# Kernel optimization log

Measured on AMD Instinct MI355X. Metric: run time of the kernel, lower is better.

## Reference

```python
import jax, jax.numpy as jnp
import numpy as np

EPS = 1e-6
K = 20
B, N = 4, 4096
HID, CDIM = 128, 64


def vn_lin(W, x):
    # W: [Cout, Cin], x: [B, Cin, 3, ...] -> [B, Cout, 3, ...]
    return jnp.einsum('oc,bc...->bo...', W, x)


def vn_leaky(x, d, ns=0.0):
    # vector-neuron leaky ReLU: reflect the part of x anti-aligned with direction d
    dot = jnp.sum(x * d, axis=2, keepdims=True)
    dsq = jnp.sum(d * d, axis=2, keepdims=True)
    return ns * x + (1.0 - ns) * jnp.where(dot >= 0, x, x - (dot / (dsq + EPS)) * d)


def vn_max_pool(x, Wd):
    # pool over the LAST axis, picking per-(b,c) the vector maximizing <x, d>
    d = vn_lin(Wd, x)
    dot = jnp.sum(x * d, axis=2, keepdims=True)            # [B,C,1,...,L]
    idx = jnp.broadcast_to(jnp.argmax(dot, axis=-1), x.shape[:-1])
    return jnp.take_along_axis(x, idx[..., None], axis=-1)[..., 0]


def graph_feature_cross(pts, k):
    # pts: [B, N, 3] -> [B, 3ch, 3vec, N, k] with channels (nbr-x, x, cross(nbr,x))
    sq = jnp.sum(pts * pts, axis=-1)
    inner = jnp.einsum('bnd,bmd->bnm', pts, pts)
    neg_dist = 2.0 * inner - sq[:, :, None] - sq[:, None, :]
    _, idx = jax.lax.top_k(neg_dist, k)                     # [B, N, k]
    nbr = jax.vmap(lambda p, i: p[i])(pts, idx)             # [B, N, k, 3]
    x = jnp.broadcast_to(pts[:, :, None, :], nbr.shape)
    cross = jnp.cross(nbr, x, axis=-1)
    feat = jnp.stack([nbr - x, x, cross], axis=3)           # [B, N, k, 3ch, 3vec]
    return jnp.transpose(feat, (0, 3, 4, 1, 2))


def resblock(x, a0, f0, a1, f1, sc):
    net = vn_lin(f0, vn_leaky(x, vn_lin(a0, x)))
    dx = vn_lin(f1, vn_leaky(net, vn_lin(a1, net)))
    return vn_lin(sc, x) + dx


def _init(key, shape, fan_in):
    return jax.random.normal(key, shape, jnp.float32) / np.sqrt(fan_in)


def setup_inputs():
    key = jax.random.key(0)
    ks = jax.random.split(key, 14)
    return {
        'pc': jax.random.normal(ks[0], (B, N, 3), jnp.float32),
        'conv_Wf': _init(ks[1], (64, 3), 3),
        'conv_Wd': _init(ks[2], (64, 3), 3),
        'pool_pos_Wd': _init(ks[3], (64, 64), 64),
        'fc_pos_W': _init(ks[4], (2 * HID, 64), 64),
        'blk_a0': _init(ks[5], (5, 2 * HID, 2 * HID), 2 * HID),
        'blk_f0': _init(ks[6], (5, HID, 2 * HID), 2 * HID),
        'blk_a1': _init(ks[7], (5, HID, HID), HID),
        'blk_f1': _init(ks[8], (5, HID, HID), HID),
        'blk_sc': _init(ks[9], (5, HID, 2 * HID), 2 * HID),
        'pool_Wd': _init(ks[10], (5, HID, HID), HID),
        'actc_Wd': _init(ks[11], (HID, HID), HID),
        'fcc_W': _init(ks[12], (CDIM, HID), HID),
    }


def reference(pc, conv_Wf, conv_Wd, pool_pos_Wd, fc_pos_W, blk_a0, blk_f0, blk_a1, blk_f1, blk_sc, pool_Wd, actc_Wd, fcc_W):
    b = pc.shape[0]
    feat = graph_feature_cross(pc, K)                         # [B,3,3,N,k]
    net = vn_leaky(vn_lin(conv_Wf, feat), vn_lin(conv_Wd, feat))  # [B,64,3,N,k]
    net = vn_max_pool(net, pool_pos_Wd)                       # [B,64,3,N] (pool over k)
    net = vn_lin(fc_pos_W, net)                               # [B,256,3,N]
    for i in range(5):
        net = resblock(net, blk_a0[i], blk_f0[i], blk_a1[i], blk_f1[i], blk_sc[i])  # [B,128,3,N]
        if i < 4:
            pooled = vn_max_pool(net, pool_Wd[i])             # [B,128,3] (pool over N)
            net = jnp.concatenate([net, jnp.broadcast_to(pooled[..., None], net.shape)], axis=1)
    net = vn_max_pool(net, pool_Wd[4])                        # [B,128,3]
    c = vn_lin(fcc_W, vn_leaky(net, vn_lin(actc_Wd, net)))    # [B,64,3]
    return c.reshape(b, -1)                                   # [B,192]
```

## Files before the change

### kernel.cpp

```cpp
#include <hip/hip_runtime.h>
#include <hip/hip_bf16.h>
#include <math.h>

#define NPTS 4096
#define NB 4
#define KNN 20
#define NCOLS (3*NPTS)
#define NEG_INF (-__builtin_huge_valf())
#define DNEG_INF (-__builtin_huge_val())

typedef _Float16 f16x8 __attribute__((ext_vector_type(8)));
typedef _Float16 f16x4 __attribute__((ext_vector_type(4)));
typedef float f32x4 __attribute__((ext_vector_type(4)));

#define WOFF_FC 0
#define WOFF_A0 16384
#define WOFF_F0 344064
#define WOFF_A1 507904
#define WOFF_F1 589824
#define WOFF_SC 671744
#define WOFF_PW 835584
#define WTOT    917504

__global__ __launch_bounds__(512) void knn_kernel(const float* __restrict__ pc,
                                                  int* __restrict__ idx) {
  __shared__ float pts[NPTS*3];
  __shared__ double msv[2][8];
  __shared__ int    msn[2][8];
  int b = blockIdx.x >> 10;
  int rowblk = blockIdx.x & 1023;
  const float* pb = pc + (size_t)b*NPTS*3;
  for (int i = threadIdx.x; i < NPTS*3; i += 512) pts[i] = pb[i];
  __syncthreads();
  int wave = threadIdx.x >> 6;
  int lane = threadIdx.x & 63;
  int row  = wave >> 1;
  int half = wave & 1;
  int l128 = half*64 + lane;
  int n = rowblk*4 + row;
  double pn0 = pts[n*3+0], pn1 = pts[n*3+1], pn2 = pts[n*3+2];
  double sqn = pn0*pn0 + pn1*pn1 + pn2*pn2;
  double nd[32];
#pragma unroll
  for (int j = 0; j < 32; ++j) {
    int m = j*128 + l128;
    double q0 = pts[m*3+0], q1 = pts[m*3+1], q2 = pts[m*3+2];
    double inner = pn0*q0 + pn1*q1 + pn2*q2;
    double sqm = q0*q0 + q1*q1 + q2*q2;
    nd[j] = 2.0*inner - sqn - sqm;
  }
  double gm[2]; int gj[2];
#pragma unroll
  for (int g = 0; g < 2; ++g) {
    double v = nd[g*16]; int jb = g*16;
#pragma unroll
    for (int jj = 1; jj < 16; ++jj) {
      int j = g*16 + jj;
      bool take = nd[j] > v;
      v = take ? nd[j] : v;
      jb = take ? j : jb;
    }
    gm[g] = v; gj[g] = jb;
  }
  int* orow = idx + ((size_t)b*NPTS + n)*KNN;
  for (int t = 0; t < KNN; ++t) {
    double bv = gm[0]; int bj = gj[0];
    if (gm[1] > bv) { bv = gm[1]; bj = gj[1]; }
    int bm = bj*128 + l128;
#pragma unroll
    for (int s = 1; s < 64; s <<= 1) {
      double ov = __shfl_xor(bv, s, 64);
      int om = __shfl_xor(bm, s, 64);
      bool take = (ov > bv) || (ov == bv && om < bm);
      bv = take ? ov : bv;
      bm = take ? om : bm;
    }
    if (lane == 0) { msv[t&1][wave] = bv; msn[t&1][wave] = bm; }
    __syncthreads();
    {
      double pv = msv[t&1][wave^1]; int pm = msn[t&1][wave^1];
      bool take = (pv > bv) || (pv == bv && pm < bm);
      bv = take ? pv : bv;
      bm = take ? pm : bm;
    }
    if (half == 0 && lane == 0) orow[t] = bm;
    if (t < KNN-1) {
      int vic_l128 = bm & 127;
      int jw = bm >> 7;
      int vic_half = vic_l128 >> 6;
      if (vic_half == half) {
        bool iswl = (l128 == vic_l128);
        int gw = jw >> 4;
#define REBUILD(G) { \
  _Pragma("unroll") \
  for (int jj = 0; jj < 16; ++jj) { \
    int j = (G)*16 + jj; \
    if (iswl && j == jw) nd[j] = DNEG_INF; \
  } \
  double v = nd[(G)*16]; int jb = (G)*16; \
  _Pragma("unroll") \
  for (int jj = 1; jj < 16; ++jj) { \
    int j = (G)*16 + jj; \
    bool take = nd[j] > v; \
    v = take ? nd[j] : v; \
    jb = take ? j : jb; \
  } \
  gm[G] = v; gj[G] = jb; \
}
        if (gw == 0) REBUILD(0)
        else         REBUILD(1)
#undef REBUILD
      }
    }
  }
}

#define ECH 5
__global__ __launch_bounds__(128) void edgeconv_kernel(
    const float* __restrict__ pc, const int* __restrict__ knnidx,
    const float* __restrict__ Wf, const float* __restrict__ Wd,
    const float* __restrict__ Wp, float* __restrict__ outp) {
  __shared__ float xls[2*ECH*3*64];
  int wave = threadIdx.x >> 6, lane = threadIdx.x & 63;
  int pid0 = blockIdx.x * 2;
  int b = pid0 >> 12;
  int n = (pid0 & (NPTS-1)) + wave;
  const float* pb = pc + (size_t)b*NPTS*3;
  int c = lane;
  float wrow[64];
#pragma unroll
  for (int j = 0; j < 64; ++j) wrow[j] = Wp[c*64 + j];
  float wf0 = Wf[c*3+0], wf1 = Wf[c*3+1], wf2 = Wf[c*3+2];
  float wd0 = Wd[c*3+0], wd1 = Wd[c*3+1], wd2 = Wd[c*3+2];
  float f9[9];
#pragma unroll
  for (int i = 0; i < 9; ++i) f9[i] = 0.0f;
  if (lane < KNN) {
    int j = knnidx[((size_t)b*NPTS + n)*KNN + lane];
    float q0 = pb[j*3+0], q1 = pb[j*3+1], q2 = pb[j*3+2];
    float x0 = pb[n*3+0], x1 = pb[n*3+1], x2 = pb[n*3+2];
    f9[0] = q0-x0; f9[1] = q1-x1; f9[2] = q2-x2;
    f9[3] = x0;    f9[4] = x1;    f9[5] = x2;
    f9[6] = q1*x2 - q2*x1;
    f9[7] = q2*x0 - q0*x2;
    f9[8] = q0*x1 - q1*x0;
  }
  float* xw = &xls[wave*ECH*3*64];
  double bdot = DNEG_INF;
  float bx0 = 0.f, bx1 = 0.f, bx2 = 0.f;
  for (int k0 = 0; k0 < KNN; k0 += ECH) {
    for (int kc = 0; kc < ECH; ++kc) {
      int kk = k0 + kc;
      float fch[9];
#pragma unroll
      for (int i = 0; i < 9; ++i) fch[i] = __shfl(f9[i], kk, 64);
      float fv[3], dv[3];
#pragma unroll
      for (int v = 0; v < 3; ++v) {
        fv[v] = wf0*fch[v] + wf1*fch[3+v] + wf2*fch[6+v];
        dv[v] = wd0*fch[v] + wd1*fch[3+v] + wd2*fch[6+v];
      }
      float dot = fv[0]*dv[0] + fv[1]*dv[1] + fv[2]*dv[2];
      if (dot < 0.0f) {
        float dsq = dv[0]*dv[0] + dv[1]*dv[1] + dv[2]*dv[2];
        float s = dot / (dsq + 1e-6f);
        fv[0] -= s*dv[0]; fv[1] -= s*dv[1]; fv[2] -= s*dv[2];
      }
      xw[(0*ECH+kc)*64 + c] = fv[0];
      xw[(1*ECH+kc)*64 + c] = fv[1];
      xw[(2*ECH+kc)*64 + c] = fv[2];
    }
    for (int kc = 0; kc < ECH; ++kc) {
      float a0 = 0.f, a1 = 0.f, a2 = 0.f;
#pragma unroll
      for (int j = 0; j < 64; j += 4) {
        float4 v0 = *(const float4*)&xw[(0*ECH+kc)*64 + j];
        float4 v1 = *(const float4*)&xw[(1*ECH+kc)*64 + j];
        float4 v2 = *(const float4*)&xw[(2*ECH+kc)*64 + j];
        a0 += wrow[j]*v0.x + wrow[j+1]*v0.y + wrow[j+2]*v0.z + wrow[j+3]*v0.w;
        a1 += wrow[j]*v1.x + wrow[j+1]*v1.y + wrow[j+2]*v1.z + wrow[j+3]*v1.w;
        a2 += wrow[j]*v2.x + wrow[j+1]*v2.y + wrow[j+2]*v2.z + wrow[j+3]*v2.w;
      }
      float xc0 = xw[(0*ECH+kc)*64 + c];
      float xc1 = xw[(1*ECH+kc)*64 + c];
      float xc2 = xw[(2*ECH+kc)*64 + c];
      double dd = (double)xc0*a0 + (double)xc1*a1 + (double)xc2*a2;
      bool take = dd > bdot;
      bdot = take ? dd : bdot;
      bx0 = take ? xc0 : bx0;
      bx1 = take ? xc1 : bx1;
      bx2 = take ? xc2 : bx2;
    }
  }
  outp[((size_t)b*NCOLS + 0*NPTS + n)*64 + c] = bx0;
  outp[((size_t)b*NCOLS + 1*NPTS + n)*64 + c] = bx1;
  outp[((size_t)b*NCOLS + 2*NPTS + n)*64 + c] = bx2;
}

__global__ __launch_bounds__(256) void wsplit_kernel(
    const float* __restrict__ fc, const float* __restrict__ a0,
    const float* __restrict__ f0, const float* __restrict__ a1,
    const float* __restrict__ f1, const float* __restrict__ sc,
    const float* __restrict__ pw, _Float16* __restrict__ outp) {
  int i = blockIdx.x*256 + threadIdx.x;
  const float* src; int off;
  if      (i < WOFF_A0) { src = fc; off = WOFF_FC; }
  else if (i < WOFF_F0) { src = a0; off = WOFF_A0; }
  else if (i < WOFF_A1) { src = f0; off = WOFF_F0; }
  else if (i < WOFF_F1) { src = a1; off = WOFF_A1; }
  else if (i < WOFF_SC) { src = f1; off = WOFF_F1; }
  else if (i < WOFF_PW) { src = sc; off = WOFF_SC; }
  else                  { src = pw; off = WOFF_PW; }
  float w = src[i - off];
  _Float16 h = (_Float16)w;
  outp[i] = h;
  outp[i + WTOT] = (_Float16)(w - (float)h);
}

__global__ __launch_bounds__(256) void bias_kernel(
    const float* __restrict__ W, const float* __restrict__ pooled,
    float* __restrict__ bias, int Cout, int Wstride) {
  int id = blockIdx.x*256 + threadIdx.x;
  int co = id % Cout; int t = id / Cout;
  int v = t % 3; int b = t / 3;
  double acc = 0.0;
  const float* wr = W + (size_t)co*Wstride + 128;
  const float* pp = pooled + (size_t)b*384 + v;
#pragma unroll 4
  for (int c = 0; c < 128; ++c)
    acc += (double)wr[c] * (double)pp[c*3];
  bias[id] = (float)acc;
}

#define LDP 40
__global__ __launch_bounds__(256) void gemm_mfma(
    const _Float16* __restrict__ Wh, const _Float16* __restrict__ Wl,
    const float* __restrict__ X, const float* __restrict__ Z,
    const float* __restrict__ bias, float* __restrict__ Y,
    int Cin, int Wstride, int ldX, int ldY, int ldZ, int addZ, int Cbias) {
  __shared__ __align__(16) _Float16 Ah[64*LDP];
  __shared__ __align__(16) _Float16 Al[64*LDP];
  __shared__ __align__(16) _Float16 Bh[128*LDP];
  __shared__ __align__(16) _Float16 Bl[128*LDP];
  int b = blockIdx.z;
  int sp0 = blockIdx.x * 64;
  int co0 = blockIdx.y * 128;
  const float* Xb = X + ((size_t)b*NCOLS + sp0) * ldX;
  int t = threadIdx.x;
  int arow = t >> 2, akoff = (t & 3) * 8;
  int brow = t >> 1, bkoff = (t & 1) * 16;
  int wid = t >> 6, lane = t & 63;
  int wr = (wid >> 1) * 32, wc = (wid & 1) * 64;
  int lrow = lane & 15, lk = (lane >> 4) * 8;
  f32x4 acc[2][4];
#pragma unroll
  for (int f = 0; f < 2; ++f)
#pragma unroll
    for (int g = 0; g < 4; ++g)
#pragma unroll
      for (int r = 0; r < 4; ++r) acc[f][g][r] = 0.0f;

  for (int k0 = 0; k0 < Cin; k0 += 32) {
    const float* xs = Xb + (size_t)arow*ldX + k0 + akoff;
    float xv[8];
    *(float4*)&xv[0] = *(const float4*)&xs[0];
    *(float4*)&xv[4] = *(const float4*)&xs[4];
    _Float16 xh[8], xl[8];
#pragma unroll
    for (int j = 0; j < 8; ++j) {
      _Float16 h = (_Float16)xv[j];
      xh[j] = h; xl[j] = (_Float16)(xv[j] - (float)h);
    }
    *(f16x8*)&Ah[arow*LDP + akoff] = *(f16x8*)&xh[0];
    *(f16x8*)&Al[arow*LDP + akoff] = *(f16x8*)&xl[0];
    const _Float16* whs = Wh + (size_t)(co0 + brow)*Wstride + k0 + bkoff;
    const _Float16* wls = Wl + (size_t)(co0 + brow)*Wstride + k0 + bkoff;
    *(f16x8*)&Bh[brow*LDP + bkoff]     = *(const f16x8*)&whs[0];
    *(f16x8*)&Bh[brow*LDP + bkoff + 8] = *(const f16x8*)&whs[8];
    *(f16x8*)&Bl[brow*LDP + bkoff]     = *(const f16x8*)&wls[0];
    *(f16x8*)&Bl[brow*LDP + bkoff + 8] = *(const f16x8*)&wls[8];
    __syncthreads();
    f16x8 ah[2], al[2], bh[4], bl[4];
#pragma unroll
    for (int f = 0; f < 2; ++f) {
      ah[f] = *(f16x8*)&Ah[(wr + f*16 + lrow)*LDP + lk];
      al[f] = *(f16x8*)&Al[(wr + f*16 + lrow)*LDP + lk];
    }
#pragma unroll
    for (int g = 0; g < 4; ++g) {
      bh[g] = *(f16x8*)&Bh[(wc + g*16 + lrow)*LDP + lk];
      bl[g] = *(f16x8*)&Bl[(wc + g*16 + lrow)*LDP + lk];
    }
#pragma unroll
    for (int f = 0; f < 2; ++f)
#pragma unroll
      for (int g = 0; g < 4; ++g) {
        acc[f][g] = __builtin_amdgcn_mfma_f32_16x16x32_f16(ah[f], bh[g], acc[f][g], 0, 0, 0);
        acc[f][g] = __builtin_amdgcn_mfma_f32_16x16x32_f16(ah[f], bl[g], acc[f][g], 0, 0, 0);
        acc[f][g] = __builtin_amdgcn_mfma_f32_16x16x32_f16(al[f], bh[g], acc[f][g], 0, 0, 0);
      }
    __syncthreads();
  }
  int lr0 = (lane >> 4) * 4, lc = lane & 15;
  float badd[4] = {0.f, 0.f, 0.f, 0.f};
  if (bias) {
    int v = sp0 >> 12;
    const float* brow2 = bias + ((size_t)b*3 + v)*Cbias;
#pragma unroll
    for (int g = 0; g < 4; ++g) badd[g] = brow2[co0 + wc + g*16 + lc];
  }
#pragma unroll
  for (int f = 0; f < 2; ++f)
#pragma unroll
    for (int g = 0; g < 4; ++g)
#pragma unroll
      for (int r = 0; r < 4; ++r) {
        int sp = sp0 + wr + f*16 + lr0 + r;
        int co = co0 + wc + g*16 + lc;
        float val = acc[f][g][r] + badd[g];
        if (addZ) val += Z[((size_t)b*NCOLS + sp)*ldZ + co];
        Y[((size_t)b*NCOLS + sp)*ldY + co] = val;
      }
}

template<int FM>
__global__ __launch_bounds__(256) void gemm_leaky(
    const _Float16* __restrict__ Wh, const _Float16* __restrict__ Wl,
    const float* __restrict__ X, const float* __restrict__ pooled,
    const float* __restrict__ bias, float* __restrict__ Y,
    int Cin, int Wstride, int ldX, int ldY, int Cbias) {
  constexpr int BM = FM*32;
  __shared__ __align__(16) _Float16 Ah[BM*LDP];
  __shared__ __align__(16) _Float16 Al[BM*LDP];
  __shared__ __align__(16) _Float16 Bh[128*LDP];
  __shared__ __align__(16) _Float16 Bl[128*LDP];
  int b = blockIdx.z;
  int n0 = blockIdx.x * BM;
  int co0 = blockIdx.y * 128;
  int t = threadIdx.x;
  constexpr int APT = BM/8;
  constexpr int TPR = 32/APT;
  int arow = t / TPR, akoff = (t % TPR) * APT;
  int brow = t >> 1, bkoff = (t & 1) * 16;
  int wid = t >> 6, lane = t & 63;
  int wr = (wid >> 1) * (BM/2), wc = (wid & 1) * 64;
  int lrow = lane & 15, lk = (lane >> 4) * 8;
  f32x4 acc[3][FM][4];
#pragma unroll
  for (int v = 0; v < 3; ++v)
#pragma unroll
    for (int f = 0; f < FM; ++f)
#pragma unroll
      for (int g = 0; g < 4; ++g)
#pragma unroll
        for (int r = 0; r < 4; ++r) acc[v][f][g][r] = 0.0f;

  for (int v = 0; v < 3; ++v) {
    const float* Xb = X + ((size_t)b*NCOLS + (size_t)v*NPTS + n0) * ldX;
    for (int k0 = 0; k0 < Cin; k0 += 32) {
      const float* xs = Xb + (size_t)arow*ldX + k0 + akoff;
      float xv[APT];
#pragma unroll
      for (int j = 0; j < APT; j += 4)
        *(float4*)&xv[j] = *(const float4*)&xs[j];
      _Float16 xh[APT], xl[APT];
#pragma unroll
      for (int j = 0; j < APT; ++j) {
        _Float16 h = (_Float16)xv[j];
        xh[j] = h; xl[j] = (_Float16)(xv[j] - (float)h);
      }
      if (APT == 8) {
        *(f16x8*)&Ah[arow*LDP + akoff] = *(f16x8*)&xh[0];
        *(f16x8*)&Al[arow*LDP + akoff] = *(f16x8*)&xl[0];
      } else {
        *(f16x4*)&Ah[arow*LDP + akoff] = *(f16x4*)&xh[0];
        *(f16x4*)&Al[arow*LDP + akoff] = *(f16x4*)&xl[0];
      }
      const _Float16* whs = Wh + (size_t)(co0 + brow)*Wstride + k0 + bkoff;
      const _Float16* wls = Wl + (size_t)(co0 + brow)*Wstride + k0 + bkoff;
      *(f16x8*)&Bh[brow*LDP + bkoff]     = *(const f16x8*)&whs[0];
      *(f16x8*)&Bh[brow*LDP + bkoff + 8] = *(const f16x8*)&whs[8];
      *(f16x8*)&Bl[brow*LDP + bkoff]     = *(const f16x8*)&wls[0];
      *(f16x8*)&Bl[brow*LDP + bkoff + 8] = *(const f16x8*)&wls[8];
      __syncthreads();
      f16x8 ah[FM], al[FM], bh[4], bl[4];
#pragma unroll
      for (int f = 0; f < FM; ++f) {
        ah[f] = *(f16x8*)&Ah[(wr + f*16 + lrow)*LDP + lk];
        al[f] = *(f16x8*)&Al[(wr + f*16 + lrow)*LDP + lk];
      }
#pragma unroll
      for (int g = 0; g < 4; ++g) {
        bh[g] = *(f16x8*)&Bh[(wc + g*16 + lrow)*LDP + lk];
        bl[g] = *(f16x8*)&Bl[(wc + g*16 + lrow)*LDP + lk];
      }
#pragma unroll
      for (int f = 0; f < FM; ++f)
#pragma unroll
        for (int g = 0; g < 4; ++g) {
          acc[v][f][g] = __builtin_amdgcn_mfma_f32_16x16x32_f16(ah[f], bh[g], acc[v][f][g], 0, 0, 0);
          acc[v][f][g] = __builtin_amdgcn_mfma_f32_16x16x32_f16(ah[f], bl[g], acc[v][f][g], 0, 0, 0);
          acc[v][f][g] = __builtin_amdgcn_mfma_f32_16x16x32_f16(al[f], bh[g], acc[v][f][g], 0, 0, 0);
        }
      __syncthreads();
    }
  }
  int lr0 = (lane >> 4) * 4, lc = lane & 15;
  float badd[3][4];
#pragma unroll
  for (int v = 0; v < 3; ++v)
#pragma unroll
    for (int g = 0; g < 4; ++g) {
      badd[v][g] = bias ? bias[((size_t)b*3 + v)*Cbias + co0 + wc + g*16 + lc] : 0.0f;
    }
  bool xfromX = (pooled == nullptr) || (co0 < 128);
#pragma unroll
  for (int f = 0; f < FM; ++f)
#pragma unroll
    for (int g = 0; g < 4; ++g)
#pragma unroll
      for (int r = 0; r < 4; ++r) {
        int n = n0 + wr + f*16 + lr0 + r;
        int co = co0 + wc + g*16 + lc;
        float x0, x1, x2;
        if (xfromX) {
          x0 = X[((size_t)b*NCOLS + 0*NPTS + n)*ldX + co];
          x1 = X[((size_t)b*NCOLS + 1*NPTS + n)*ldX + co];
          x2 = X[((size_t)b*NCOLS + 2*NPTS + n)*ldX + co];
        } else {
          const float* pp = pooled + (size_t)b*384 + (co - 128)*3;
          x0 = pp[0]; x1 = pp[1]; x2 = pp[2];
        }
        float d0 = acc[0][f][g][r] + badd[0][g];
        float d1 = acc[1][f][g][r] + badd[1][g];
        float d2 = acc[2][f][g][r] + badd[2][g];
        float dot = x0*d0 + x1*d1 + x2*d2;
        float u0 = x0, u1 = x1, u2 = x2;
        if (dot < 0.0f) {
          float dsq = d0*d0 + d1*d1 + d2*d2;
          float s = dot / (dsq + 1e-6f);
          u0 = x0 - s*d0; u1 = x1 - s*d1; u2 = x2 - s*d2;
        }
        Y[((size_t)b*NCOLS + 0*NPTS + n)*ldY + co] = u0;
        Y[((size_t)b*NCOLS + 1*NPTS + n)*ldY + co] = u1;
        Y[((size_t)b*NCOLS + 2*NPTS + n)*ldY + co] = u2;
      }
}

__global__ __launch_bounds__(256) void pool1_kernel(
    const float* __restrict__ Net, const float* __restrict__ Dm,
    double* __restrict__ pv, int* __restrict__ pn, int ldN, int ldD) {
  __shared__ double sv[256];
  __shared__ int sn[256];
  int b = blockIdx.y;
  int n0 = blockIdx.x * 256;
  int c = threadIdx.x & 127;
  int half = threadIdx.x >> 7;
  double bv = DNEG_INF; int bn = 0x7fffffff;
  for (int i = 0; i < 128; ++i) {
    int n = n0 + 2*i + half;
    size_t r0 = ((size_t)b*NCOLS + n);
    double dot =
        (double)Net[(r0)*ldN + c]              * (double)Dm[(r0)*ldD + c]
      + (double)Net[(r0 + NPTS)*ldN + c]       * (double)Dm[(r0 + NPTS)*ldD + c]
      + (double)Net[(r0 + 2*NPTS)*ldN + c]     * (double)Dm[(r0 + 2*NPTS)*ldD + c];
    if (dot > bv) { bv = dot; bn = n; }
  }
  sv[threadIdx.x] = bv; sn[threadIdx.x] = bn;
  __syncthreads();
  if (half == 0) {
    double v1 = sv[threadIdx.x + 128]; int n1 = sn[threadIdx.x + 128];
    if (v1 > bv || (v1 == bv && n1 < bn)) { bv = v1; bn = n1; }
    pv[((size_t)b*16 + blockIdx.x)*128 + c] = bv;
    pn[((size_t)b*16 + blockIdx.x)*128 + c] = bn;
  }
}

__global__ __launch_bounds__(128) void pool2_kernel(
    const double* __restrict__ pv, const int* __restrict__ pn,
    const float* __restrict__ Net, float* __restrict__ pooled, int ldN) {
  int b = blockIdx.x, c = threadIdx.x;
  double bv = DNEG_INF; int bn = 0x7fffffff;
  for (int ch = 0; ch < 16; ++ch) {
    double v = pv[((size_t)b*16 + ch)*128 + c];
    int nn = pn[((size_t)b*16 + ch)*128 + c];
    if (v > bv || (v == bv && nn < bn)) { bv = v; bn = nn; }
  }
#pragma unroll
  for (int v = 0; v < 3; ++v)
    pooled[(size_t)b*384 + c*3 + v] = Net[((size_t)b*NCOLS + v*NPTS + bn)*ldN + c];
}

__global__ __launch_bounds__(128) void head_kernel(
    const float* __restrict__ pooled, const float* __restrict__ Wa,
    const float* __restrict__ Wc, float* __restrict__ out) {
  __shared__ float xp[128*3], up[128*3];
  int b = blockIdx.x, c = threadIdx.x;
#pragma unroll
  for (int v = 0; v < 3; ++v) xp[c*3+v] = pooled[(size_t)b*384 + c*3 + v];
  __syncthreads();
  float a0 = 0.f, a1 = 0.f, a2 = 0.f;
  for (int j = 0; j < 128; ++j) {
    float w = Wa[c*128+j];
    a0 += w*xp[j*3+0]; a1 += w*xp[j*3+1]; a2 += w*xp[j*3+2];
  }
  float x0 = xp[c*3+0], x1 = xp[c*3+1], x2 = xp[c*3+2];
  float dot = x0*a0 + x1*a1 + x2*a2;
  float u0 = x0, u1 = x1, u2 = x2;
  if (dot < 0.0f) {
    float dsq = a0*a0 + a1*a1 + a2*a2;
    float s = dot / (dsq + 1e-6f);
    u0 = x0 - s*a0; u1 = x1 - s*a1; u2 = x2 - s*a2;
  }
  up[c*3+0] = u0; up[c*3+1] = u1; up[c*3+2] = u2;
  __syncthreads();
  if (c < 64) {
    float o0 = 0.f, o1 = 0.f, o2 = 0.f;
    for (int j = 0; j < 128; ++j) {
      float w = Wc[c*128+j];
      o0 += w*up[j*3+0]; o1 += w*up[j*3+1]; o2 += w*up[j*3+2];
    }
    out[(size_t)b*192 + c*3 + 0] = o0;
    out[(size_t)b*192 + c*3 + 1] = o1;
    out[(size_t)b*192 + c*3 + 2] = o2;
  }
}

extern "C" void kernel_launch(void* const* d_in, const int* in_sizes, int n_in,
                              void* d_out, int out_size, void* d_ws, size_t ws_size,
                              hipStream_t stream) {
  const float* pc    = (const float*)d_in[0];
  const float* cWf   = (const float*)d_in[1];
  const float* cWd   = (const float*)d_in[2];
  const float* pposW = (const float*)d_in[3];
  const float* fcW   = (const float*)d_in[4];
  const float* ba0   = (const float*)d_in[5];
  const float* bf0   = (const float*)d_in[6];
  const float* ba1   = (const float*)d_in[7];
  const float* bf1   = (const float*)d_in[8];
  const float* bscW  = (const float*)d_in[9];
  const float* pWd   = (const float*)d_in[10];
  const float* aWd   = (const float*)d_in[11];
  const float* fccW  = (const float*)d_in[12];
  float* out = (float*)d_out;
  char* ws = (char*)d_ws;
  const size_t MB = 1u << 20;
  const size_t KB = 1u << 10;
  int*      idxb   = (int*)(ws);
  float*    X1     = (float*)(ws + 2*MB);
  float*    X2     = (float*)(ws + 52*MB);
  float*    conv   = (float*)(ws + 52*MB);
  float*    T      = (float*)(ws + 102*MB);
  float*    T2     = T;
  float*    DX     = (float*)(ws + 126*MB);
  float*    Hn     = (float*)(ws + 152*MB);
  float*    pooled = (float*)(ws + 178*MB);
  double*   pv     = (double*)(ws + 178*MB + 64*KB);
  int*      pn     = (int*)(ws + 178*MB + 128*KB);
  float*    biasA  = (float*)(ws + 178*MB + 256*KB);
  float*    biasS  = (float*)(ws + 178*MB + 320*KB);
  _Float16* Wsp    = (_Float16*)(ws + 179*MB);
  _Float16* WspLo  = Wsp + WTOT;

  wsplit_kernel<<<WTOT/256, 256, 0, stream>>>(fcW, ba0, bf0, ba1, bf1, bscW, pWd, Wsp);
  knn_kernel<<<NB*NPTS/4, 512, 0, stream>>>(pc, idxb);
  edgeconv_kernel<<<NB*NPTS/2, 128, 0, stream>>>(pc, idxb, cWf, cWd, pposW, conv);
  gemm_mfma<<<dim3(192, 2, NB), 256, 0, stream>>>(Wsp + WOFF_FC, WspLo + WOFF_FC,
      conv, nullptr, nullptr, X1, 64, 64, 64, 256, 0, 0, 0);

  float* Xin = X1; float* Xout = X2;
  for (int i = 0; i < 5; ++i) {
    const _Float16* a0h = Wsp   + WOFF_A0 + (size_t)i*65536;
    const _Float16* a0l = WspLo + WOFF_A0 + (size_t)i*65536;
    const _Float16* f0h = Wsp   + WOFF_F0 + (size_t)i*32768;
    const _Float16* f0l = WspLo + WOFF_F0 + (size_t)i*32768;
    const _Float16* a1h = Wsp   + WOFF_A1 + (size_t)i*16384;
    const _Float16* a1l = WspLo + WOFF_A1 + (size_t)i*16384;
    const _Float16* f1h = Wsp   + WOFF_F1 + (size_t)i*16384;
    const _Float16* f1l = WspLo + WOFF_F1 + (size_t)i*16384;
    const _Float16* sch = Wsp   + WOFF_SC + (size_t)i*32768;
    const _Float16* scl = WspLo + WOFF_SC + (size_t)i*32768;
    const _Float16* pwh = Wsp   + WOFF_PW + (size_t)i*16384;
    const _Float16* pwl = WspLo + WOFF_PW + (size_t)i*16384;
    int KA = (i == 0) ? 256 : 128;
    const float* bA = (i == 0) ? nullptr : biasA;
    const float* bS = (i == 0) ? nullptr : biasS;
    const float* lp = (i == 0) ? nullptr : pooled;
    if (i > 0) {
      bias_kernel<<<NB*3*256/256,256,0,stream>>>(ba0 + (size_t)i*65536, pooled, biasA, 256, 256);
      bias_kernel<<<NB*3*128/256,256,0,stream>>>(bscW + (size_t)i*32768, pooled, biasS, 128, 256);
    }
    gemm_leaky<2><<<dim3(NPTS/64, 2, NB), 256, 0, stream>>>(a0h, a0l, Xin, lp, bA, T,
        KA, 256, 256, 256, 256);
    gemm_mfma<<<dim3(192,1,NB),256,0,stream>>>(f0h, f0l, T, nullptr, nullptr, Hn,
        256, 256, 256, 128, 0, 0, 0);
    gemm_leaky<1><<<dim3(NPTS/32, 1, NB), 256, 0, stream>>>(a1h, a1l, Hn, nullptr, nullptr, T2,
        128, 128, 128, 128, 0);
    gemm_mfma<<<dim3(192,1,NB),256,0,stream>>>(f1h, f1l, T2, nullptr, nullptr, DX,
        128, 128, 128, 128, 0, 0, 0);
    gemm_mfma<<<dim3(192,1,NB),256,0,stream>>>(sch, scl, Xin, DX, bS, Xout,
        KA, 256, 256, 256, 128, 1, 128);
    gemm_mfma<<<dim3(192,1,NB),256,0,stream>>>(pwh, pwl, Xout, nullptr, nullptr, Hn,
        128, 128, 256, 128, 0, 0, 0);
    pool1_kernel<<<dim3(16,NB),256,0,stream>>>(Xout, Hn, pv, pn, 256, 128);
    pool2_kernel<<<NB,128,0,stream>>>(pv, pn, Xout, pooled, 256);
    if (i < 4) { float* tmp = Xin; Xin = Xout; Xout = tmp; }
  }
  head_kernel<<<NB,128,0,stream>>>(pooled, aWd, fccW, out);
}
```

Before: 1.549 ms.

## Fuse residual f1 and shortcut GEMMs, merge bias kernels, widen pool1 grid

Adds a gemm_dual kernel that runs the f1 projection and the shortcut projection as one concatenated-K GEMM accumulating into a single output. This removes the DX intermediate write and read plus one launch. The two bias kernels are merged into one launch. pool1 now splits N into 64 chunks instead of 16 for more parallelism, at the cost of a longer serial reduction in pool2.

```diff
diff --git a/kernel.cpp b/kernel.cpp
--- a/kernel.cpp
+++ b/kernel.cpp
@@ -217,19 +217,23 @@
   outp[i + WTOT] = (_Float16)(w - (float)h);
 }
 
-__global__ __launch_bounds__(256) void bias_kernel(
-    const float* __restrict__ W, const float* __restrict__ pooled,
-    float* __restrict__ bias, int Cout, int Wstride) {
+__global__ __launch_bounds__(256) void bias2_kernel(
+    const float* __restrict__ Wa0, const float* __restrict__ Wsc,
+    const float* __restrict__ pooled,
+    float* __restrict__ biasA, float* __restrict__ biasS) {
   int id = blockIdx.x*256 + threadIdx.x;
-  int co = id % Cout; int t = id / Cout;
+  const float* W; float* dst; int Cout; int idx;
+  if (id < NB*3*256) { W = Wa0; dst = biasA; Cout = 256; idx = id; }
+  else               { W = Wsc; dst = biasS; Cout = 128; idx = id - NB*3*256; }
+  int co = idx % Cout; int t = idx / Cout;
   int v = t % 3; int b = t / 3;
   double acc = 0.0;
-  const float* wr = W + (size_t)co*Wstride + 128;
+  const float* wr = W + (size_t)co*256 + 128;
   const float* pp = pooled + (size_t)b*384 + v;
 #pragma unroll 4
   for (int c = 0; c < 128; ++c)
     acc += (double)wr[c] * (double)pp[c*3];
-  bias[id] = (float)acc;
+  dst[idx] = (float)acc;
 }
 
 #define LDP 40
@@ -320,6 +324,103 @@
         float val = acc[f][g][r] + badd[g];
         if (addZ) val += Z[((size_t)b*NCOLS + sp)*ldZ + co];
         Y[((size_t)b*NCOLS + sp)*ldY + co] = val;
+      }
+}
+
+__global__ __launch_bounds__(256) void gemm_dual(
+    const _Float16* __restrict__ W1h, const _Float16* __restrict__ W1l,
+    const _Float16* __restrict__ W2h, const _Float16* __restrict__ W2l,
+    const float* __restrict__ X1, const float* __restrict__ X2s,
+    const float* __restrict__ bias, float* __restrict__ Y,
+    int K2, int ldY, int Cbias) {
+  __shared__ __align__(16) _Float16 Ah[64*LDP];
+  __shared__ __align__(16) _Float16 Al[64*LDP];
+  __shared__ __align__(16) _Float16 Bh[128*LDP];
+  __shared__ __align__(16) _Float16 Bl[128*LDP];
+  int b = blockIdx.z;
+  int sp0 = blockIdx.x * 64;
+  int co0 = blockIdx.y * 128;
+  int t = threadIdx.x;
+  int arow = t >> 2, akoff = (t & 3) * 8;
+  int brow = t >> 1, bkoff = (t & 1) * 16;
+  int wid = t >> 6, lane = t & 63;
+  int wr = (wid >> 1) * 32, wc = (wid & 1) * 64;
+  int lrow = lane & 15, lk = (lane >> 4) * 8;
+  f32x4 acc[2][4];
+#pragma unroll
+  for (int f = 0; f < 2; ++f)
+#pragma unroll
+    for (int g = 0; g < 4; ++g)
+#pragma unroll
+      for (int r = 0; r < 4; ++r) acc[f][g][r] = 0.0f;
+
+  int Ktot = 128 + K2;
+  for (int k0 = 0; k0 < Ktot; k0 += 32) {
+    const float* xs;
+    const _Float16 *whs, *wls;
+    if (k0 < 128) {
+      xs  = X1 + ((size_t)b*NCOLS + sp0 + arow)*128 + k0 + akoff;
+      whs = W1h + (size_t)(co0 + brow)*128 + k0 + bkoff;
+      wls = W1l + (size_t)(co0 + brow)*128 + k0 + bkoff;
+    } else {
+      xs  = X2s + ((size_t)b*NCOLS + sp0 + arow)*256 + (k0-128) + akoff;
+      whs = W2h + (size_t)(co0 + brow)*256 + (k0-128) + bkoff;
+      wls = W2l + (size_t)(co0 + brow)*256 + (k0-128) + bkoff;
+    }
+    float xv[8];
+    *(float4*)&xv[0] = *(const float4*)&xs[0];
+    *(float4*)&xv[4] = *(const float4*)&xs[4];
+    _Float16 xh[8], xl[8];
+#pragma unroll
+    for (int j = 0; j < 8; ++j) {
+      _Float16 h = (_Float16)xv[j];
+      xh[j] = h; xl[j] = (_Float16)(xv[j] - (float)h);
+    }
+    *(f16x8*)&Ah[arow*LDP + akoff] = *(f16x8*)&xh[0];
+    *(f16x8*)&Al[arow*LDP + akoff] = *(f16x8*)&xl[0];
+    *(f16x8*)&Bh[brow*LDP + bkoff]     = *(const f16x8*)&whs[0];
+    *(f16x8*)&Bh[brow*LDP + bkoff + 8] = *(const f16x8*)&whs[8];
+    *(f16x8*)&Bl[brow*LDP + bkoff]     = *(const f16x8*)&wls[0];
+    *(f16x8*)&Bl[brow*LDP + bkoff + 8] = *(const f16x8*)&wls[8];
+    __syncthreads();
+    f16x8 ah[2], al[2], bh[4], bl[4];
+#pragma unroll
+    for (int f = 0; f < 2; ++f) {
+      ah[f] = *(f16x8*)&Ah[(wr + f*16 + lrow)*LDP + lk];
+      al[f] = *(f16x8*)&Al[(wr + f*16 + lrow)*LDP + lk];
+    }
+#pragma unroll
+    for (int g = 0; g < 4; ++g) {
+      bh[g] = *(f16x8*)&Bh[(wc + g*16 + lrow)*LDP + lk];
+      bl[g] = *(f16x8*)&Bl[(wc + g*16 + lrow)*LDP + lk];
+    }
+#pragma unroll
+    for (int f = 0; f < 2; ++f)
+#pragma unroll
+      for (int g = 0; g < 4; ++g) {
+        acc[f][g] = __builtin_amdgcn_mfma_f32_16x16x32_f16(ah[f], bh[g], acc[f][g], 0, 0, 0);
+        acc[f][g] = __builtin_amdgcn_mfma_f32_16x16x32_f16(ah[f], bl[g], acc[f][g], 0, 0, 0);
+        acc[f][g] = __builtin_amdgcn_mfma_f32_16x16x32_f16(al[f], bh[g], acc[f][g], 0, 0, 0);
+      }
+    __syncthreads();
+  }
+  int lr0 = (lane >> 4) * 4, lc = lane & 15;
+  float badd[4] = {0.f, 0.f, 0.f, 0.f};
+  if (bias) {
+    int v = sp0 >> 12;
+    const float* brow2 = bias + ((size_t)b*3 + v)*Cbias;
+#pragma unroll
+    for (int g = 0; g < 4; ++g) badd[g] = brow2[co0 + wc + g*16 + lc];
+  }
+#pragma unroll
+  for (int f = 0; f < 2; ++f)
+#pragma unroll
+    for (int g = 0; g < 4; ++g)
+#pragma unroll
+      for (int r = 0; r < 4; ++r) {
+        int sp = sp0 + wr + f*16 + lr0 + r;
+        int co = co0 + wc + g*16 + lc;
+        Y[((size_t)b*NCOLS + sp)*ldY + co] = acc[f][g][r] + badd[g];
       }
 }
 
@@ -453,11 +554,11 @@
   __shared__ double sv[256];
   __shared__ int sn[256];
   int b = blockIdx.y;
-  int n0 = blockIdx.x * 256;
+  int n0 = blockIdx.x * 64;
   int c = threadIdx.x & 127;
   int half = threadIdx.x >> 7;
   double bv = DNEG_INF; int bn = 0x7fffffff;
-  for (int i = 0; i < 128; ++i) {
+  for (int i = 0; i < 32; ++i) {
     int n = n0 + 2*i + half;
     size_t r0 = ((size_t)b*NCOLS + n);
     double dot =
@@ -471,8 +572,8 @@
   if (half == 0) {
     double v1 = sv[threadIdx.x + 128]; int n1 = sn[threadIdx.x + 128];
     if (v1 > bv || (v1 == bv && n1 < bn)) { bv = v1; bn = n1; }
-    pv[((size_t)b*16 + blockIdx.x)*128 + c] = bv;
-    pn[((size_t)b*16 + blockIdx.x)*128 + c] = bn;
+    pv[((size_t)b*64 + blockIdx.x)*128 + c] = bv;
+    pn[((size_t)b*64 + blockIdx.x)*128 + c] = bn;
   }
 }
 
@@ -481,9 +582,9 @@
     const float* __restrict__ Net, float* __restrict__ pooled, int ldN) {
   int b = blockIdx.x, c = threadIdx.x;
   double bv = DNEG_INF; int bn = 0x7fffffff;
-  for (int ch = 0; ch < 16; ++ch) {
-    double v = pv[((size_t)b*16 + ch)*128 + c];
-    int nn = pn[((size_t)b*16 + ch)*128 + c];
+  for (int ch = 0; ch < 64; ++ch) {
+    double v = pv[((size_t)b*64 + ch)*128 + c];
+    int nn = pn[((size_t)b*64 + ch)*128 + c];
     if (v > bv || (v == bv && nn < bn)) { bv = v; bn = nn; }
   }
 #pragma unroll
@@ -552,13 +653,12 @@
   float*    conv   = (float*)(ws + 52*MB);
   float*    T      = (float*)(ws + 102*MB);
   float*    T2     = T;
-  float*    DX     = (float*)(ws + 126*MB);
   float*    Hn     = (float*)(ws + 152*MB);
   float*    pooled = (float*)(ws + 178*MB);
-  double*   pv     = (double*)(ws + 178*MB + 64*KB);
-  int*      pn     = (int*)(ws + 178*MB + 128*KB);
-  float*    biasA  = (float*)(ws + 178*MB + 256*KB);
-  float*    biasS  = (float*)(ws + 178*MB + 320*KB);
+  double*   pv     = (double*)(ws + 178*MB + 16*KB);
+  int*      pn     = (int*)(ws + 178*MB + 288*KB);
+  float*    biasA  = (float*)(ws + 178*MB + 448*KB);
+  float*    biasS  = (float*)(ws + 178*MB + 512*KB);
   _Float16* Wsp    = (_Float16*)(ws + 179*MB);
   _Float16* WspLo  = Wsp + WTOT;
 
@@ -587,8 +687,8 @@
     const float* bS = (i == 0) ? nullptr : biasS;
     const float* lp = (i == 0) ? nullptr : pooled;
     if (i > 0) {
-      bias_kernel<<<NB*3*256/256,256,0,stream>>>(ba0 + (size_t)i*65536, pooled, biasA, 256, 256);
-      bias_kernel<<<NB*3*128/256,256,0,stream>>>(bscW + (size_t)i*32768, pooled, biasS, 128, 256);
+      bias2_kernel<<<(NB*3*384+255)/256,256,0,stream>>>(
+          ba0 + (size_t)i*65536, bscW + (size_t)i*32768, pooled, biasA, biasS);
     }
     gemm_leaky<2><<<dim3(NPTS/64, 2, NB), 256, 0, stream>>>(a0h, a0l, Xin, lp, bA, T,
         KA, 256, 256, 256, 256);
@@ -596,13 +696,11 @@
         256, 256, 256, 128, 0, 0, 0);
     gemm_leaky<1><<<dim3(NPTS/32, 1, NB), 256, 0, stream>>>(a1h, a1l, Hn, nullptr, nullptr, T2,
         128, 128, 128, 128, 0);
-    gemm_mfma<<<dim3(192,1,NB),256,0,stream>>>(f1h, f1l, T2, nullptr, nullptr, DX,
-        128, 128, 128, 128, 0, 0, 0);
-    gemm_mfma<<<dim3(192,1,NB),256,0,stream>>>(sch, scl, Xin, DX, bS, Xout,
-        KA, 256, 256, 256, 128, 1, 128);
+    gemm_dual<<<dim3(192,1,NB),256,0,stream>>>(f1h, f1l, sch, scl, T2, Xin, bS, Xout,
+        KA, 256, 128);
     gemm_mfma<<<dim3(192,1,NB),256,0,stream>>>(pwh, pwl, Xout, nullptr, nullptr, Hn,
         128, 128, 256, 128, 0, 0, 0);
-    pool1_kernel<<<dim3(16,NB),256,0,stream>>>(Xout, Hn, pv, pn, 256, 128);
+    pool1_kernel<<<dim3(64,NB),256,0,stream>>>(Xout, Hn, pv, pn, 256, 128);
     pool2_kernel<<<NB,128,0,stream>>>(pv, pn, Xout, pooled, 256);
     if (i < 4) { float* tmp = Xin; Xin = Xout; Xout = tmp; }
   }
```

Result: faster. 1.340 ms (-13.5%).
